# Optimization experiments

Hardware: AMD Instinct MI355X
Metric: run time of the kernel (lower is better)

The kernel has to match this reference:

```python
import jax, jax.numpy as jnp
import numpy as np

A = 0.4          # sigma: uniform noise half-width Uniform(-A, A)
THRESHOLD = 1.0
TAU_INV = 0.5    # module stores 1.0 / tau with tau = 2.0


@jax.custom_vjp
def spike(v, unif):
    # StochasticST.forward: bernoulli(clamp((v + A) / (2A), 0, 1))
    p = jnp.clip((v + A) / (2.0 * A), 0.0, 1.0)
    return (unif < p).astype(v.dtype)


def _spike_fwd(v, unif):
    return spike(v, unif), v


def _spike_bwd(v, g):
    # StochasticST.backward: straight-through window [-A, A] with slope 1/(2A)
    surrogate = ((v >= -A) & (v <= A)).astype(g.dtype) * (1.0 / (2.0 * A))
    return (g * surrogate, jnp.zeros(v.shape, g.dtype))


spike.defvjp(_spike_fwd, _spike_bwd)


def setup_inputs() -> dict:
    key = jax.random.key(0)
    k1, k2, k3 = jax.random.split(key, 3)
    B, T, N = 32, 16, 65536
    x = jax.random.normal(k1, (B, T, N), dtype=jnp.float32)
    # pre-sampled uniform_(-A, A) noise (one draw per timestep/element)
    noise = jax.random.uniform(k2, (B, T, N), dtype=jnp.float32, minval=-A, maxval=A)
    # pre-sampled uniforms driving the bernoulli spike draw
    unif = jax.random.uniform(k3, (B, T, N), dtype=jnp.float32)
    return {"x": x, "noise": noise, "unif": unif}


def reference(x, noise, unif):
    # x: [B, T, N] -> scan over T with membrane state u: [B, N]
    xt = jnp.swapaxes(x, 0, 1)      # [T, B, N]
    nt = jnp.swapaxes(noise, 0, 1)  # [T, B, N]
    rt = jnp.swapaxes(unif, 0, 1)   # [T, B, N]
    u0 = jnp.zeros((x.shape[0], x.shape[2]), x.dtype)

    def step(u, inp):
        xi, ni, ri = inp
        u = TAU_INV * u + xi          # leaky integrate
        u = u - ni                    # u += -Uniform(-A, A) noise injection
        o = spike(u - THRESHOLD, ri)  # stochastic threshold spike
        u = u * (1.0 - o)             # hard reset where spiked
        return u, o

    _, o = jax.lax.scan(step, u0, (xt, nt, rt))
    return jnp.swapaxes(o, 0, 1)  # [B, T, N] spike train
```

## Files before the change

kernel.cpp:

```cpp
#include <hip/hip_runtime.h>


namespace {

constexpr int B = 32;
constexpr int T = 16;
constexpr int N = 65536;
constexpr int N4 = N / 4;
constexpr int N4_SHIFT = 14;

constexpr float SIGMA = 0.4f;
constexpr float TWO_SIGMA = 0.8f;
constexpr float THRESHOLD = 1.0f;
constexpr float TAU_INV = 0.5f;

__device__ __forceinline__ float lif_step(float& u, float xi, float ni, float ri) {
    u = TAU_INV * u + xi;
    u = u - ni;
    float v = u - THRESHOLD;
    float p = (v + SIGMA) / TWO_SIGMA;
    p = fminf(fmaxf(p, 0.0f), 1.0f);
    float o = (ri < p) ? 1.0f : 0.0f;
    u = u * (1.0f - o);
    return o;
}

__global__ __launch_bounds__(256) void snn_scan_kernel(
    const float4* __restrict__ x,
    const float4* __restrict__ noise,
    const float4* __restrict__ unif,
    float4* __restrict__ out)
{
    const int tid = blockIdx.x * blockDim.x + threadIdx.x;
    const int b  = tid >> N4_SHIFT;
    const int nc = tid & (N4 - 1);

    int idx = b * T * N4 + nc;
    float4 u = make_float4(0.0f, 0.0f, 0.0f, 0.0f);

    for (int t = 0; t < T; ++t, idx += N4) {
        const float4 xi = x[idx];
        const float4 ni = noise[idx];
        const float4 ri = unif[idx];
        float4 o;
        o.x = lif_step(u.x, xi.x, ni.x, ri.x);
        o.y = lif_step(u.y, xi.y, ni.y, ri.y);
        o.z = lif_step(u.z, xi.z, ni.z, ri.z);
        o.w = lif_step(u.w, xi.w, ni.w, ri.w);
        out[idx] = o;
    }
}

}

extern "C" void kernel_launch(void* const* d_in, const int* in_sizes, int n_in,
                              void* d_out, int out_size, void* d_ws, size_t ws_size,
                              hipStream_t stream) {
    const float4* x     = (const float4*)d_in[0];
    const float4* noise = (const float4*)d_in[1];
    const float4* unif  = (const float4*)d_in[2];
    float4* out         = (float4*)d_out;

    const int threads_total = B * N4;
    const int block = 256;
    const int grid = threads_total / block;

    snn_scan_kernel<<<grid, block, 0, stream>>>(x, noise, unif, out);
}
```

Before: 401.3 us.

## Process two batch rows per thread with software-prefetched next-timestep loads

Each thread now scans two independent batch chains (b and b+16) and loads the next timestep's inputs before computing the current step. This aims to raise memory-level parallelism and hide load latency in the serial scan over T. It halves the grid size and raises register use, which reduces the number of resident waves available to hide latency.

```diff
diff --git a/kernel.cpp b/kernel.cpp
--- a/kernel.cpp
+++ b/kernel.cpp
@@ -8,6 +8,7 @@
 constexpr int N = 65536;
 constexpr int N4 = N / 4;
 constexpr int N4_SHIFT = 14;
+constexpr int HALF = (B / 2) * T * N4;
 
 constexpr float SIGMA = 0.4f;
 constexpr float TWO_SIGMA = 0.8f;
@@ -25,6 +26,16 @@
     return o;
 }
 
+__device__ __forceinline__ float4 lif_step4(float4& u, const float4& xi,
+                                            const float4& ni, const float4& ri) {
+    float4 o;
+    o.x = lif_step(u.x, xi.x, ni.x, ri.x);
+    o.y = lif_step(u.y, xi.y, ni.y, ri.y);
+    o.z = lif_step(u.z, xi.z, ni.z, ri.z);
+    o.w = lif_step(u.w, xi.w, ni.w, ri.w);
+    return o;
+}
+
 __global__ __launch_bounds__(256) void snn_scan_kernel(
     const float4* __restrict__ x,
     const float4* __restrict__ noise,
@@ -32,23 +43,34 @@
     float4* __restrict__ out)
 {
     const int tid = blockIdx.x * blockDim.x + threadIdx.x;
-    const int b  = tid >> N4_SHIFT;
+    const int b0 = tid >> N4_SHIFT;
     const int nc = tid & (N4 - 1);
 
-    int idx = b * T * N4 + nc;
-    float4 u = make_float4(0.0f, 0.0f, 0.0f, 0.0f);
+    int idx0 = b0 * T * N4 + nc;
+    int idx1 = idx0 + HALF;
 
-    for (int t = 0; t < T; ++t, idx += N4) {
-        const float4 xi = x[idx];
-        const float4 ni = noise[idx];
-        const float4 ri = unif[idx];
-        float4 o;
-        o.x = lif_step(u.x, xi.x, ni.x, ri.x);
-        o.y = lif_step(u.y, xi.y, ni.y, ri.y);
-        o.z = lif_step(u.z, xi.z, ni.z, ri.z);
-        o.w = lif_step(u.w, xi.w, ni.w, ri.w);
-        out[idx] = o;
+    float4 u0 = make_float4(0.f, 0.f, 0.f, 0.f);
+    float4 u1 = make_float4(0.f, 0.f, 0.f, 0.f);
+
+    float4 cx0 = x[idx0], cn0 = noise[idx0], cr0 = unif[idx0];
+    float4 cx1 = x[idx1], cn1 = noise[idx1], cr1 = unif[idx1];
+
+    for (int t = 0; t < T - 1; ++t) {
+        const int nidx0 = idx0 + N4;
+        const int nidx1 = idx1 + N4;
+        float4 nx0 = x[nidx0], nn0 = noise[nidx0], nr0 = unif[nidx0];
+        float4 nx1 = x[nidx1], nn1 = noise[nidx1], nr1 = unif[nidx1];
+
+        out[idx0] = lif_step4(u0, cx0, cn0, cr0);
+        out[idx1] = lif_step4(u1, cx1, cn1, cr1);
+
+        cx0 = nx0; cn0 = nn0; cr0 = nr0;
+        cx1 = nx1; cn1 = nn1; cr1 = nr1;
+        idx0 = nidx0; idx1 = nidx1;
     }
+
+    out[idx0] = lif_step4(u0, cx0, cn0, cr0);
+    out[idx1] = lif_step4(u1, cx1, cn1, cr1);
 }
 
 }
@@ -61,7 +83,7 @@
     const float4* unif  = (const float4*)d_in[2];
     float4* out         = (float4*)d_out;
 
-    const int threads_total = B * N4;
+    const int threads_total = (B / 2) * N4;
     const int block = 256;
     const int grid = threads_total / block;
 
```

New measurement: 394.2 us. Within noise of the previous version (-1.8%).
